# Kernel optimization log

Measured on AMD Instinct MI355X. Metric: run time of the kernel, lower is better.

Reference implementation:

```python
import jax, jax.numpy as jnp
from jax import lax
import numpy as np

B, T, C = 2048, 512, 32  # batch, max_seq_len, num_tags


def setup_inputs() -> dict:
    key = jax.random.key(0)
    k1, k2, k3, k4 = jax.random.split(key, 4)
    logits = jax.random.normal(k1, (B, T, C), dtype=jnp.float32)
    sequence_length = jax.random.randint(k2, (B,), 1, T + 1, dtype=jnp.int32)
    labels = jax.random.randint(k3, (B, T), 0, C, dtype=jnp.int32)
    # learned CRF transition matrix (orthogonal init approximated by normal)
    transitions = jax.random.normal(k4, (C, C), dtype=jnp.float32)
    return dict(logits=logits, sequence_length=sequence_length,
                labels=labels, transitions=transitions)


def _viterbi_decode(logits, transitions, seq_len):
    """tfa_text.crf_decode: returns highest-scoring tag sequence [B, T] int32."""
    Bn, Tn, Cn = logits.shape
    identity_bp = jnp.arange(Cn, dtype=jnp.int32)[None, :]  # carries tag through padding

    def fwd(state, xs):  # state: [B, C] viterbi scores
        logit_t, t = xs
        scores = state[:, :, None] + transitions[None]       # [B, C_prev, C_cur]
        cand = logit_t + jnp.max(scores, axis=1)             # [B, C]
        bp = jnp.argmax(scores, axis=1).astype(jnp.int32)    # [B, C] best prev tag
        active = (t < seq_len)[:, None]
        return (jnp.where(active, cand, state),
                jnp.where(active, bp, identity_bp))

    xs = (jnp.swapaxes(logits[:, 1:], 0, 1), jnp.arange(1, Tn))
    final_state, bps = lax.scan(fwd, logits[:, 0], xs)       # bps: [T-1, B, C]
    last_tag = jnp.argmax(final_state, axis=-1).astype(jnp.int32)  # [B]

    def back(tag, bp):  # tag at t+1 -> tag at t
        prev = jnp.take_along_axis(bp, tag[:, None], axis=1)[:, 0]
        return prev, tag

    first_tag, later_tags = lax.scan(back, last_tag, bps, reverse=True)
    tags = jnp.concatenate([first_tag[None], later_tags], axis=0).T  # [B, T]
    valid = jnp.arange(Tn)[None, :] < seq_len[:, None]
    return jnp.where(valid, tags, 0)


def _crf_log_likelihood(logits, labels, transitions, seq_len):
    """tfa_text.crf_log_likelihood: per-example log-likelihood [B]."""
    Bn, Tn, Cn = logits.shape

    # --- log partition via forward algorithm ---
    def fwd(alpha, xs):
        logit_t, t = xs
        new = jax.nn.logsumexp(alpha[:, :, None] + transitions[None], axis=1) + logit_t
        active = (t < seq_len)[:, None]
        return jnp.where(active, new, alpha), None

    xs = (jnp.swapaxes(logits[:, 1:], 0, 1), jnp.arange(1, Tn))
    alpha, _ = lax.scan(fwd, logits[:, 0], xs)
    log_norm = jax.nn.logsumexp(alpha, axis=-1)  # [B]

    # --- score of gold label sequence ---
    pos = jnp.arange(Tn)
    mask = (pos[None, :] < seq_len[:, None]).astype(logits.dtype)          # [B, T]
    unary = jnp.sum(
        jnp.take_along_axis(logits, labels[..., None], axis=2)[..., 0] * mask,
        axis=1)
    pair_mask = (pos[None, :-1] < (seq_len - 1)[:, None]).astype(logits.dtype)
    binary = jnp.sum(transitions[labels[:, :-1], labels[:, 1:]] * pair_mask, axis=1)

    return unary + binary - log_norm


def reference(logits, sequence_length, labels, transitions):
    # training=True path: labels clamped to >= 0 (already non-negative here)
    labels = jnp.maximum(labels, 0)
    decode_tags = _viterbi_decode(logits, transitions, sequence_length)
    log_likelihood = _crf_log_likelihood(logits, labels, transitions, sequence_length)
    loss = jnp.mean(-log_likelihood)  # recorded via add_loss in the original
    return decode_tags, loss
```

## Files before the change

### kernel.cpp

```cpp
#include <hip/hip_runtime.h>
#include <math.h>

#define BB 2048
#define TT 512
#define CC 32

#if __has_builtin(__builtin_amdgcn_exp2f)
#define EXP2F __builtin_amdgcn_exp2f
#else
#define EXP2F exp2f
#endif
#if __has_builtin(__builtin_amdgcn_logf)
#define LOG2F __builtin_amdgcn_logf
#else
#define LOG2F log2f
#endif

#define LOG2E 1.4426950408889634f
#define LN2   0.6931471805599453f

__global__ void zero_loss_kernel(float* __restrict__ out) {
  if (threadIdx.x == 0) out[(size_t)BB * TT] = 0.0f;
}

#define ROR(dst, src, K)                                                     \
  dst = __int_as_float(__builtin_amdgcn_update_dpp(                          \
      0, __float_as_int(src), 0x120 | (K), 0xF, 0xF, false));

__global__ __launch_bounds__(128, 4) void crf_kernel(
    const float* __restrict__ logits,
    const int*   __restrict__ seqlen,
    const int*   __restrict__ labels,
    const float* __restrict__ trans,
    float*       __restrict__ out)
{
  __shared__ __align__(16) unsigned char bp_s[(TT - 1) * CC];
  __shared__ __align__(16) float avs[CC];
  __shared__ unsigned char tag_s[TT];

  const int lane = threadIdx.x & 63;
  const int wv   = threadIdx.x >> 6;
  const int b    = blockIdx.x;

  const int len = seqlen[b];
  const float* lg = logits + (size_t)b * TT * CC;
  const size_t bT = (size_t)b * TT;

  if (wv == 0) {
    const int c = lane & 31;
    const int h = lane >> 5;

    float tr[16];
#pragma unroll
    for (int i = 0; i < 16; ++i) tr[i] = trans[(h * 16 + i) * CC + c];

    float av = lg[c];
    if (h == 0) avs[c] = av;

    const float4* avp = (const float4*)(avs + h * 16);

    const float* lgc = lg + c;
    float l0 = 0, l1 = 0, l2 = 0;
    {
      int r1 = 1 < len ? 1 : len - 1;
      int r2 = 2 < len ? 2 : len - 1;
      int r3 = 3 < len ? 3 : len - 1;
      l0 = lgc[r1 * CC]; l1 = lgc[r2 * CC]; l2 = lgc[r3 * CC];
    }

    auto vstep = [&](int t, float logit_c) {
      float pav[16];
#pragma unroll
      for (int qq = 0; qq < 4; ++qq) ((float4*)pav)[qq] = avp[qq];

      float S[16];
#pragma unroll
      for (int i = 0; i < 16; ++i) S[i] = pav[i] + tr[i];

      float m8[8];
#pragma unroll
      for (int k = 0; k < 8; ++k) m8[k] = fmaxf(S[k], S[k + 8]);
#pragma unroll
      for (int k = 0; k < 4; ++k) m8[k] = fmaxf(m8[k], m8[k + 4]);
      float best = fmaxf(fmaxf(m8[0], m8[2]), fmaxf(m8[1], m8[3]));

      int t8[16];
#pragma unroll
      for (int i = 0; i < 16; ++i) t8[i] = (S[i] == best) ? i : 63;
#pragma unroll
      for (int k = 0; k < 8; ++k) t8[k] = min(t8[k], t8[k + 8]);
#pragma unroll
      for (int k = 0; k < 4; ++k) t8[k] = min(t8[k], t8[k + 4]);
      int bi = min(min(t8[0], t8[2]), min(t8[1], t8[3]));
      int bpi = h * 16 + bi;

      float ov = __shfl_xor(best, 32);
      int   oi = __shfl_xor(bpi, 32);
      bool take = (ov > best) || (ov == best && oi < bpi);
      best = take ? ov : best;
      bpi  = take ? oi : bpi;
      av = logit_c + best;

      if (h == 0) {
        avs[c] = av;
        bp_s[(t - 1) * CC + c] = (unsigned char)bpi;
      }
    };

    int t = 1;
    int tmain = len - 3;
    for (; t < tmain; ++t) {
      float lc = l0; l0 = l1; l1 = l2;
      l2 = lgc[(t + 3) * CC];
      vstep(t, lc);
    }
    for (; t < len; ++t) {
      float lc = l0; l0 = l1; l1 = l2;
      int rn = t + 3; rn = rn < len ? rn : len - 1;
      l2 = lgc[rn * CC];
      vstep(t, lc);
    }

    float v = av; int idx = c;
#pragma unroll
    for (int d = 1; d < 32; d <<= 1) {
      float v2 = __shfl_xor(v, d, 32);
      int   i2 = __shfl_xor(idx, d, 32);
      if (v2 > v || (v2 == v && i2 < idx)) { v = v2; idx = i2; }
    }

    if (lane == 0) {
      int tag = idx;
      tag_s[len - 1] = (unsigned char)tag;
      const uint4* bp4 = (const uint4*)bp_s;
      uint4 Ra[3], Rb[3];
#pragma unroll
      for (int k = 0; k < 3; ++k) {
        int r = len - 2 - k;
        if (r >= 0) { Ra[k] = bp4[2 * r]; Rb[k] = bp4[2 * r + 1]; }
      }
      for (int tt = len - 1; tt > 0; --tt) {
        uint4 ua = Ra[0], ub = Rb[0];
        Ra[0] = Ra[1]; Rb[0] = Rb[1];
        Ra[1] = Ra[2]; Rb[1] = Rb[2];
        int r = tt - 4;
        if (r >= 0) { Ra[2] = bp4[2 * r]; Rb[2] = bp4[2 * r + 1]; }
        uint4 u4;
        u4.x = (tag & 16) ? ub.x : ua.x;
        u4.y = (tag & 16) ? ub.y : ua.y;
        u4.z = (tag & 16) ? ub.z : ua.z;
        u4.w = (tag & 16) ? ub.w : ua.w;
        unsigned lo = (tag & 8) ? u4.z : u4.x;
        unsigned hi = (tag & 8) ? u4.w : u4.y;
        unsigned u1 = (tag & 4) ? hi : lo;
        tag = (int)((u1 >> ((tag & 3) * 8)) & 0xffu);
        tag_s[tt - 1] = (unsigned char)tag;
      }
    }

#pragma unroll
    for (int j = 0; j < 8; ++j) {
      int tt = lane + 64 * j;
      float val = (tt < len) ? (float)tag_s[tt] : 0.0f;
      out[bT + tt] = val;
    }

  } else {
    const int* lab = labels + (size_t)b * TT;
    const int i = lane & 15;
    const int r = (lane >> 4) & 1;
    const int c = lane & 31;
    const int pr = (lane < 32) ? r : (1 - r);
    const int bpaddr = ((lane < 32) ? lane : (lane ^ 16)) << 2;

    float E[16];
#pragma unroll
    for (int k = 0; k < 16; ++k) {
      int p = pr * 16 + ((i - k) & 15);
      E[k] = EXP2F(trans[p * CC + c] * LOG2E);
    }

    float P   = EXP2F(lg[c] * LOG2E);
    float Acc = 0.0f;

    const float* lgc = lg + c;
    float e0 = 0, e1 = 0, e2 = 0;
    {
      int r1 = 1 < len ? 1 : len - 1;
      int r2 = 2 < len ? 2 : len - 1;
      int r3 = 3 < len ? 3 : len - 1;
      e0 = EXP2F(lgc[r1 * CC] * LOG2E);
      e1 = EXP2F(lgc[r2 * CC] * LOG2E);
      e2 = EXP2F(lgc[r3 * CC] * LOG2E);
    }

    auto fstep = [&](float el) {
      float base = __int_as_float(
          __builtin_amdgcn_ds_bpermute(bpaddr, __float_as_int(P)));
      float x;
      float a0 = base * E[0];
      ROR(x, base, 1);  float a1 = x * E[1];
      ROR(x, base, 2);  float a2 = x * E[2];
      ROR(x, base, 3);  float a3 = x * E[3];
      ROR(x, base, 4);  a0 = fmaf(x, E[4],  a0);
      ROR(x, base, 5);  a1 = fmaf(x, E[5],  a1);
      ROR(x, base, 6);  a2 = fmaf(x, E[6],  a2);
      ROR(x, base, 7);  a3 = fmaf(x, E[7],  a3);
      ROR(x, base, 8);  a0 = fmaf(x, E[8],  a0);
      ROR(x, base, 9);  a1 = fmaf(x, E[9],  a1);
      ROR(x, base, 10); a2 = fmaf(x, E[10], a2);
      ROR(x, base, 11); a3 = fmaf(x, E[11], a3);
      ROR(x, base, 12); a0 = fmaf(x, E[12], a0);
      ROR(x, base, 13); a1 = fmaf(x, E[13], a1);
      ROR(x, base, 14); a2 = fmaf(x, E[14], a2);
      ROR(x, base, 15); a3 = fmaf(x, E[15], a3);
      float part = (a0 + a1) + (a2 + a3);
      float oth  = __shfl_xor(part, 32);
      float s    = part + oth;
      P = el * s;
    };

    auto renorm = [&]() {
      float m = P;
#pragma unroll
      for (int d = 1; d < 32; d <<= 1) m = fmaxf(m, __shfl_xor(m, d, 32));
      int e = (int)(__float_as_uint(m) >> 23) - 127;
      P = ldexpf(P, -e);
      Acc += (float)e;
    };

    int t = 1;
    int tmain = len - 3;
    for (; t < tmain; ++t) {
      float ec = e0; e0 = e1; e1 = e2;
      e2 = EXP2F(lgc[(t + 3) * CC] * LOG2E);
      fstep(ec);
      if ((t & 3) == 0) renorm();
    }
    for (; t < len; ++t) {
      float ec = e0; e0 = e1; e1 = e2;
      int rn = t + 3; rn = rn < len ? rn : len - 1;
      e2 = EXP2F(lgc[rn * CC] * LOG2E);
      fstep(ec);
      if ((t & 3) == 0) renorm();
    }

    float uacc = 0.0f, bacc = 0.0f;
#pragma unroll
    for (int j = 0; j < 8; ++j) {
      int tt = lane + 64 * j;
      if (tt < len) {
        int lt = lab[tt];
        uacc += lg[tt * CC + lt];
        if (tt + 1 < len) {
          int ln = lab[tt + 1];
          bacc += trans[lt * CC + ln];
        }
      }
    }
#pragma unroll
    for (int d = 32; d >= 1; d >>= 1) {
      uacc += __shfl_xor(uacc, d);
      bacc += __shfl_xor(bacc, d);
    }

    float ss = P;
#pragma unroll
    for (int d = 1; d < 32; d <<= 1) ss += __shfl_xor(ss, d, 32);
    float log_norm = LN2 * (Acc + LOG2F(ss));

    if (lane == 0) {
      float ll = uacc + bacc - log_norm;
      atomicAdd(out + (size_t)BB * TT, -ll * (1.0f / BB));
    }
  }
}

extern "C" void kernel_launch(void* const* d_in, const int* in_sizes, int n_in,
                              void* d_out, int out_size, void* d_ws, size_t ws_size,
                              hipStream_t stream) {
  const float* logits = (const float*)d_in[0];
  const int*   seqlen = (const int*)d_in[1];
  const int*   labels = (const int*)d_in[2];
  const float* trans  = (const float*)d_in[3];
  float* out = (float*)d_out;

  zero_loss_kernel<<<1, 64, 0, stream>>>(out);
  crf_kernel<<<dim3(BB), dim3(128), 0, stream>>>(logits, seqlen, labels, trans, out);
}
```

Before: 435.8 us.

## Sort sequences by length and pair long with short per block for load balance

Adds a single-block schedule kernel that counting-sorts batch indices by sequence length in descending order into a workspace permutation. The CRF kernel then launches half as many blocks, and each block processes sequence k and sequence BB-1-k back to back, so every block does roughly equal serial work. This targets the tail imbalance of variable-length sequential scans. It costs an extra tiny kernel launch, serialized sort work, and fewer concurrent blocks, which may lower latency hiding. The new path only runs when a workspace is provided.

```diff
diff --git a/kernel.cpp b/kernel.cpp
--- a/kernel.cpp
+++ b/kernel.cpp
@@ -23,6 +23,31 @@
   if (threadIdx.x == 0) out[(size_t)BB * TT] = 0.0f;
 }
 
+__global__ void schedule_kernel(const int* __restrict__ seqlen,
+                                int* __restrict__ perm,
+                                float* __restrict__ out) {
+  __shared__ int s[TT];
+  __shared__ int off[TT];
+  const int tid = threadIdx.x;
+  if (tid == 0) out[(size_t)BB * TT] = 0.0f;
+  s[tid] = 0;
+  __syncthreads();
+  for (int b = tid; b < BB; b += TT) atomicAdd(&s[seqlen[b] - 1], 1);
+  __syncthreads();
+  for (int d = 1; d < TT; d <<= 1) {
+    int v = s[tid] + ((tid + d < TT) ? s[tid + d] : 0);
+    __syncthreads();
+    s[tid] = v;
+    __syncthreads();
+  }
+  off[tid] = (tid + 1 < TT) ? s[tid + 1] : 0;
+  __syncthreads();
+  for (int b = tid; b < BB; b += TT) {
+    int pos = atomicAdd(&off[seqlen[b] - 1], 1);
+    perm[pos] = b;
+  }
+}
+
 #define ROR(dst, src, K)                                                     \
   dst = __int_as_float(__builtin_amdgcn_update_dpp(                          \
       0, __float_as_int(src), 0x120 | (K), 0xF, 0xF, false));
@@ -32,7 +57,8 @@
     const int*   __restrict__ seqlen,
     const int*   __restrict__ labels,
     const float* __restrict__ trans,
-    float*       __restrict__ out)
+    float*       __restrict__ out,
+    const int*   __restrict__ perm)
 {
   __shared__ __align__(16) unsigned char bp_s[(TT - 1) * CC];
   __shared__ __align__(16) float avs[CC];
@@ -40,11 +66,10 @@
 
   const int lane = threadIdx.x & 63;
   const int wv   = threadIdx.x >> 6;
-  const int b    = blockIdx.x;
-
-  const int len = seqlen[b];
-  const float* lg = logits + (size_t)b * TT * CC;
-  const size_t bT = (size_t)b * TT;
+  const int k    = blockIdx.x;
+
+  const int bs0 = perm ? perm[k] : k;
+  const int bs1 = perm ? perm[BB - 1 - k] : -1;
 
   if (wv == 0) {
     const int c = lane & 31;
@@ -54,119 +79,126 @@
 #pragma unroll
     for (int i = 0; i < 16; ++i) tr[i] = trans[(h * 16 + i) * CC + c];
 
-    float av = lg[c];
-    if (h == 0) avs[c] = av;
-
     const float4* avp = (const float4*)(avs + h * 16);
 
-    const float* lgc = lg + c;
-    float l0 = 0, l1 = 0, l2 = 0;
-    {
-      int r1 = 1 < len ? 1 : len - 1;
-      int r2 = 2 < len ? 2 : len - 1;
-      int r3 = 3 < len ? 3 : len - 1;
-      l0 = lgc[r1 * CC]; l1 = lgc[r2 * CC]; l2 = lgc[r3 * CC];
+    for (int sq = 0; sq < 2; ++sq) {
+      const int b = sq ? bs1 : bs0;
+      if (b < 0) break;
+      const int len = seqlen[b];
+      const float* lg = logits + (size_t)b * TT * CC;
+      const size_t bT = (size_t)b * TT;
+
+      float av = lg[c];
+      if (h == 0) avs[c] = av;
+
+      const float* lgc = lg + c;
+      float l0 = 0, l1 = 0, l2 = 0;
+      {
+        int r1 = 1 < len ? 1 : len - 1;
+        int r2 = 2 < len ? 2 : len - 1;
+        int r3 = 3 < len ? 3 : len - 1;
+        l0 = lgc[r1 * CC]; l1 = lgc[r2 * CC]; l2 = lgc[r3 * CC];
+      }
+
+      auto vstep = [&](int t, float logit_c) {
+        float pav[16];
+#pragma unroll
+        for (int qq = 0; qq < 4; ++qq) ((float4*)pav)[qq] = avp[qq];
+
+        float S[16];
+#pragma unroll
+        for (int i = 0; i < 16; ++i) S[i] = pav[i] + tr[i];
+
+        float m8[8];
+#pragma unroll
+        for (int kk = 0; kk < 8; ++kk) m8[kk] = fmaxf(S[kk], S[kk + 8]);
+#pragma unroll
+        for (int kk = 0; kk < 4; ++kk) m8[kk] = fmaxf(m8[kk], m8[kk + 4]);
+        float best = fmaxf(fmaxf(m8[0], m8[2]), fmaxf(m8[1], m8[3]));
+
+        int t8[16];
+#pragma unroll
+        for (int i = 0; i < 16; ++i) t8[i] = (S[i] == best) ? i : 63;
+#pragma unroll
+        for (int kk = 0; kk < 8; ++kk) t8[kk] = min(t8[kk], t8[kk + 8]);
+#pragma unroll
+        for (int kk = 0; kk < 4; ++kk) t8[kk] = min(t8[kk], t8[kk + 4]);
+        int bi = min(min(t8[0], t8[2]), min(t8[1], t8[3]));
+        int bpi = h * 16 + bi;
+
+        float ov = __shfl_xor(best, 32);
+        int   oi = __shfl_xor(bpi, 32);
+        bool take = (ov > best) || (ov == best && oi < bpi);
+        best = take ? ov : best;
+        bpi  = take ? oi : bpi;
+        av = logit_c + best;
+
+        if (h == 0) {
+          avs[c] = av;
+          bp_s[(t - 1) * CC + c] = (unsigned char)bpi;
+        }
+      };
+
+      int t = 1;
+      int tmain = len - 3;
+      for (; t < tmain; ++t) {
+        float lc = l0; l0 = l1; l1 = l2;
+        l2 = lgc[(t + 3) * CC];
+        vstep(t, lc);
+      }
+      for (; t < len; ++t) {
+        float lc = l0; l0 = l1; l1 = l2;
+        int rn = t + 3; rn = rn < len ? rn : len - 1;
+        l2 = lgc[rn * CC];
+        vstep(t, lc);
+      }
+
+      float v = av; int idx = c;
+#pragma unroll
+      for (int d = 1; d < 32; d <<= 1) {
+        float v2 = __shfl_xor(v, d, 32);
+        int   i2 = __shfl_xor(idx, d, 32);
+        if (v2 > v || (v2 == v && i2 < idx)) { v = v2; idx = i2; }
+      }
+
+      if (lane == 0) {
+        int tag = idx;
+        tag_s[len - 1] = (unsigned char)tag;
+        const uint4* bp4 = (const uint4*)bp_s;
+        uint4 Ra[3], Rb[3];
+#pragma unroll
+        for (int kk = 0; kk < 3; ++kk) {
+          int r = len - 2 - kk;
+          if (r >= 0) { Ra[kk] = bp4[2 * r]; Rb[kk] = bp4[2 * r + 1]; }
+        }
+        for (int tt = len - 1; tt > 0; --tt) {
+          uint4 ua = Ra[0], ub = Rb[0];
+          Ra[0] = Ra[1]; Rb[0] = Rb[1];
+          Ra[1] = Ra[2]; Rb[1] = Rb[2];
+          int r = tt - 4;
+          if (r >= 0) { Ra[2] = bp4[2 * r]; Rb[2] = bp4[2 * r + 1]; }
+          uint4 u4;
+          u4.x = (tag & 16) ? ub.x : ua.x;
+          u4.y = (tag & 16) ? ub.y : ua.y;
+          u4.z = (tag & 16) ? ub.z : ua.z;
+          u4.w = (tag & 16) ? ub.w : ua.w;
+          unsigned lo = (tag & 8) ? u4.z : u4.x;
+          unsigned hi = (tag & 8) ? u4.w : u4.y;
+          unsigned u1 = (tag & 4) ? hi : lo;
+          tag = (int)((u1 >> ((tag & 3) * 8)) & 0xffu);
+          tag_s[tt - 1] = (unsigned char)tag;
+        }
+      }
+
+#pragma unroll
+      for (int j = 0; j < 8; ++j) {
+        int tt = lane + 64 * j;
+        float val = (tt < len) ? (float)tag_s[tt] : 0.0f;
+        out[bT + tt] = val;
+      }
     }
 
-    auto vstep = [&](int t, float logit_c) {
-      float pav[16];
-#pragma unroll
-      for (int qq = 0; qq < 4; ++qq) ((float4*)pav)[qq] = avp[qq];
-
-      float S[16];
-#pragma unroll
-      for (int i = 0; i < 16; ++i) S[i] = pav[i] + tr[i];
-
-      float m8[8];
-#pragma unroll
-      for (int k = 0; k < 8; ++k) m8[k] = fmaxf(S[k], S[k + 8]);
-#pragma unroll
-      for (int k = 0; k < 4; ++k) m8[k] = fmaxf(m8[k], m8[k + 4]);
-      float best = fmaxf(fmaxf(m8[0], m8[2]), fmaxf(m8[1], m8[3]));
-
-      int t8[16];
-#pragma unroll
-      for (int i = 0; i < 16; ++i) t8[i] = (S[i] == best) ? i : 63;
-#pragma unroll
-      for (int k = 0; k < 8; ++k) t8[k] = min(t8[k], t8[k + 8]);
-#pragma unroll
-      for (int k = 0; k < 4; ++k) t8[k] = min(t8[k], t8[k + 4]);
-      int bi = min(min(t8[0], t8[2]), min(t8[1], t8[3]));
-      int bpi = h * 16 + bi;
-
-      float ov = __shfl_xor(best, 32);
-      int   oi = __shfl_xor(bpi, 32);
-      bool take = (ov > best) || (ov == best && oi < bpi);
-      best = take ? ov : best;
-      bpi  = take ? oi : bpi;
-      av = logit_c + best;
-
-      if (h == 0) {
-        avs[c] = av;
-        bp_s[(t - 1) * CC + c] = (unsigned char)bpi;
-      }
-    };
-
-    int t = 1;
-    int tmain = len - 3;
-    for (; t < tmain; ++t) {
-      float lc = l0; l0 = l1; l1 = l2;
-      l2 = lgc[(t + 3) * CC];
-      vstep(t, lc);
-    }
-    for (; t < len; ++t) {
-      float lc = l0; l0 = l1; l1 = l2;
-      int rn = t + 3; rn = rn < len ? rn : len - 1;
-      l2 = lgc[rn * CC];
-      vstep(t, lc);
-    }
-
-    float v = av; int idx = c;
-#pragma unroll
-    for (int d = 1; d < 32; d <<= 1) {
-      float v2 = __shfl_xor(v, d, 32);
-      int   i2 = __shfl_xor(idx, d, 32);
-      if (v2 > v || (v2 == v && i2 < idx)) { v = v2; idx = i2; }
-    }
-
-    if (lane == 0) {
-      int tag = idx;
-      tag_s[len - 1] = (unsigned char)tag;
-      const uint4* bp4 = (const uint4*)bp_s;
-      uint4 Ra[3], Rb[3];
-#pragma unroll
-      for (int k = 0; k < 3; ++k) {
-        int r = len - 2 - k;
-        if (r >= 0) { Ra[k] = bp4[2 * r]; Rb[k] = bp4[2 * r + 1]; }
-      }
-      for (int tt = len - 1; tt > 0; --tt) {
-        uint4 ua = Ra[0], ub = Rb[0];
-        Ra[0] = Ra[1]; Rb[0] = Rb[1];
-        Ra[1] = Ra[2]; Rb[1] = Rb[2];
-        int r = tt - 4;
-        if (r >= 0) { Ra[2] = bp4[2 * r]; Rb[2] = bp4[2 * r + 1]; }
-        uint4 u4;
-        u4.x = (tag & 16) ? ub.x : ua.x;
-        u4.y = (tag & 16) ? ub.y : ua.y;
-        u4.z = (tag & 16) ? ub.z : ua.z;
-        u4.w = (tag & 16) ? ub.w : ua.w;
-        unsigned lo = (tag & 8) ? u4.z : u4.x;
-        unsigned hi = (tag & 8) ? u4.w : u4.y;
-        unsigned u1 = (tag & 4) ? hi : lo;
-        tag = (int)((u1 >> ((tag & 3) * 8)) & 0xffu);
-        tag_s[tt - 1] = (unsigned char)tag;
-      }
-    }
-
-#pragma unroll
-    for (int j = 0; j < 8; ++j) {
-      int tt = lane + 64 * j;
-      float val = (tt < len) ? (float)tag_s[tt] : 0.0f;
-      out[bT + tt] = val;
-    }
-
   } else {
-    const int* lab = labels + (size_t)b * TT;
     const int i = lane & 15;
     const int r = (lane >> 4) & 1;
     const int c = lane & 31;
@@ -175,103 +207,114 @@
 
     float E[16];
 #pragma unroll
-    for (int k = 0; k < 16; ++k) {
-      int p = pr * 16 + ((i - k) & 15);
-      E[k] = EXP2F(trans[p * CC + c] * LOG2E);
+    for (int kk = 0; kk < 16; ++kk) {
+      int p = pr * 16 + ((i - kk) & 15);
+      E[kk] = EXP2F(trans[p * CC + c] * LOG2E);
     }
 
-    float P   = EXP2F(lg[c] * LOG2E);
-    float Acc = 0.0f;
-
-    const float* lgc = lg + c;
-    float e0 = 0, e1 = 0, e2 = 0;
-    {
-      int r1 = 1 < len ? 1 : len - 1;
-      int r2 = 2 < len ? 2 : len - 1;
-      int r3 = 3 < len ? 3 : len - 1;
-      e0 = EXP2F(lgc[r1 * CC] * LOG2E);
-      e1 = EXP2F(lgc[r2 * CC] * LOG2E);
-      e2 = EXP2F(lgc[r3 * CC] * LOG2E);
+    float loss_acc = 0.0f;
+
+    for (int sq = 0; sq < 2; ++sq) {
+      const int b = sq ? bs1 : bs0;
+      if (b < 0) break;
+      const int len = seqlen[b];
+      const float* lg = logits + (size_t)b * TT * CC;
+      const int* lab = labels + (size_t)b * TT;
+
+      float P   = EXP2F(lg[c] * LOG2E);
+      float Acc = 0.0f;
+
+      const float* lgc = lg + c;
+      float e0 = 0, e1 = 0, e2 = 0;
+      {
+        int r1 = 1 < len ? 1 : len - 1;
+        int r2 = 2 < len ? 2 : len - 1;
+        int r3 = 3 < len ? 3 : len - 1;
+        e0 = EXP2F(lgc[r1 * CC] * LOG2E);
+        e1 = EXP2F(lgc[r2 * CC] * LOG2E);
+        e2 = EXP2F(lgc[r3 * CC] * LOG2E);
+      }
+
+      auto fstep = [&](float el) {
+        float base = __int_as_float(
+            __builtin_amdgcn_ds_bpermute(bpaddr, __float_as_int(P)));
+        float x;
+        float a0 = base * E[0];
+        ROR(x, base, 1);  float a1 = x * E[1];
+        ROR(x, base, 2);  float a2 = x * E[2];
+        ROR(x, base, 3);  float a3 = x * E[3];
+        ROR(x, base, 4);  a0 = fmaf(x, E[4],  a0);
+        ROR(x, base, 5);  a1 = fmaf(x, E[5],  a1);
+        ROR(x, base, 6);  a2 = fmaf(x, E[6],  a2);
+        ROR(x, base, 7);  a3 = fmaf(x, E[7],  a3);
+        ROR(x, base, 8);  a0 = fmaf(x, E[8],  a0);
+        ROR(x, base, 9);  a1 = fmaf(x, E[9],  a1);
+        ROR(x, base, 10); a2 = fmaf(x, E[10], a2);
+        ROR(x, base, 11); a3 = fmaf(x, E[11], a3);
+        ROR(x, base, 12); a0 = fmaf(x, E[12], a0);
+        ROR(x, base, 13); a1 = fmaf(x, E[13], a1);
+        ROR(x, base, 14); a2 = fmaf(x, E[14], a2);
+        ROR(x, base, 15); a3 = fmaf(x, E[15], a3);
+        float part = (a0 + a1) + (a2 + a3);
+        float oth  = __shfl_xor(part, 32);
+        float s    = part + oth;
+        P = el * s;
+      };
+
+      auto renorm = [&]() {
+        float m = P;
+#pragma unroll
+        for (int d = 1; d < 32; d <<= 1) m = fmaxf(m, __shfl_xor(m, d, 32));
+        int e = (int)(__float_as_uint(m) >> 23) - 127;
+        P = ldexpf(P, -e);
+        Acc += (float)e;
+      };
+
+      int t = 1;
+      int tmain = len - 3;
+      for (; t < tmain; ++t) {
+        float ec = e0; e0 = e1; e1 = e2;
+        e2 = EXP2F(lgc[(t + 3) * CC] * LOG2E);
+        fstep(ec);
+        if ((t & 3) == 0) renorm();
+      }
+      for (; t < len; ++t) {
+        float ec = e0; e0 = e1; e1 = e2;
+        int rn = t + 3; rn = rn < len ? rn : len - 1;
+        e2 = EXP2F(lgc[rn * CC] * LOG2E);
+        fstep(ec);
+        if ((t & 3) == 0) renorm();
+      }
+
+      float uacc = 0.0f, bacc = 0.0f;
+#pragma unroll
+      for (int j = 0; j < 8; ++j) {
+        int tt = lane + 64 * j;
+        if (tt < len) {
+          int lt = lab[tt];
+          uacc += lg[tt * CC + lt];
+          if (tt + 1 < len) {
+            int ln = lab[tt + 1];
+            bacc += trans[lt * CC + ln];
+          }
+        }
+      }
+#pragma unroll
+      for (int d = 32; d >= 1; d >>= 1) {
+        uacc += __shfl_xor(uacc, d);
+        bacc += __shfl_xor(bacc, d);
+      }
+
+      float ss = P;
+#pragma unroll
+      for (int d = 1; d < 32; d <<= 1) ss += __shfl_xor(ss, d, 32);
+      float log_norm = LN2 * (Acc + LOG2F(ss));
+
+      loss_acc += (uacc + bacc - log_norm);
     }
 
-    auto fstep = [&](float el) {
-      float base = __int_as_float(
-          __builtin_amdgcn_ds_bpermute(bpaddr, __float_as_int(P)));
-      float x;
-      float a0 = base * E[0];
-      ROR(x, base, 1);  float a1 = x * E[1];
-      ROR(x, base, 2);  float a2 = x * E[2];
-      ROR(x, base, 3);  float a3 = x * E[3];
-      ROR(x, base, 4);  a0 = fmaf(x, E[4],  a0);
-      ROR(x, base, 5);  a1 = fmaf(x, E[5],  a1);
-      ROR(x, base, 6);  a2 = fmaf(x, E[6],  a2);
-      ROR(x, base, 7);  a3 = fmaf(x, E[7],  a3);
-      ROR(x, base, 8);  a0 = fmaf(x, E[8],  a0);
-      ROR(x, base, 9);  a1 = fmaf(x, E[9],  a1);
-      ROR(x, base, 10); a2 = fmaf(x, E[10], a2);
-      ROR(x, base, 11); a3 = fmaf(x, E[11], a3);
-      ROR(x, base, 12); a0 = fmaf(x, E[12], a0);
-      ROR(x, base, 13); a1 = fmaf(x, E[13], a1);
-      ROR(x, base, 14); a2 = fmaf(x, E[14], a2);
-      ROR(x, base, 15); a3 = fmaf(x, E[15], a3);
-      float part = (a0 + a1) + (a2 + a3);
-      float oth  = __shfl_xor(part, 32);
-      float s    = part + oth;
-      P = el * s;
-    };
-
-    auto renorm = [&]() {
-      float m = P;
-#pragma unroll
-      for (int d = 1; d < 32; d <<= 1) m = fmaxf(m, __shfl_xor(m, d, 32));
-      int e = (int)(__float_as_uint(m) >> 23) - 127;
-      P = ldexpf(P, -e);
-      Acc += (float)e;
-    };
-
-    int t = 1;
-    int tmain = len - 3;
-    for (; t < tmain; ++t) {
-      float ec = e0; e0 = e1; e1 = e2;
-      e2 = EXP2F(lgc[(t + 3) * CC] * LOG2E);
-      fstep(ec);
-      if ((t & 3) == 0) renorm();
-    }
-    for (; t < len; ++t) {
-      float ec = e0; e0 = e1; e1 = e2;
-      int rn = t + 3; rn = rn < len ? rn : len - 1;
-      e2 = EXP2F(lgc[rn * CC] * LOG2E);
-      fstep(ec);
-      if ((t & 3) == 0) renorm();
-    }
-
-    float uacc = 0.0f, bacc = 0.0f;
-#pragma unroll
-    for (int j = 0; j < 8; ++j) {
-      int tt = lane + 64 * j;
-      if (tt < len) {
-        int lt = lab[tt];
-        uacc += lg[tt * CC + lt];
-        if (tt + 1 < len) {
-          int ln = lab[tt + 1];
-          bacc += trans[lt * CC + ln];
-        }
-      }
-    }
-#pragma unroll
-    for (int d = 32; d >= 1; d >>= 1) {
-      uacc += __shfl_xor(uacc, d);
-      bacc += __shfl_xor(bacc, d);
-    }
-
-    float ss = P;
-#pragma unroll
-    for (int d = 1; d < 32; d <<= 1) ss += __shfl_xor(ss, d, 32);
-    float log_norm = LN2 * (Acc + LOG2F(ss));
-
     if (lane == 0) {
-      float ll = uacc + bacc - log_norm;
-      atomicAdd(out + (size_t)BB * TT, -ll * (1.0f / BB));
+      atomicAdd(out + (size_t)BB * TT, loss_acc * (-1.0f / BB));
     }
   }
 }
@@ -285,6 +328,14 @@
   const float* trans  = (const float*)d_in[3];
   float* out = (float*)d_out;
 
-  zero_loss_kernel<<<1, 64, 0, stream>>>(out);
-  crf_kernel<<<dim3(BB), dim3(128), 0, stream>>>(logits, seqlen, labels, trans, out);
+  if (d_ws != nullptr && ws_size >= BB * sizeof(int)) {
+    int* perm = (int*)d_ws;
+    schedule_kernel<<<1, TT, 0, stream>>>(seqlen, perm, out);
+    crf_kernel<<<dim3(BB / 2), dim3(128), 0, stream>>>(
+        logits, seqlen, labels, trans, out, perm);
+  } else {
+    zero_loss_kernel<<<1, 64, 0, stream>>>(out);
+    crf_kernel<<<dim3(BB), dim3(128), 0, stream>>>(
+        logits, seqlen, labels, trans, out, nullptr);
+  }
 }
```

Result: faster. 421.4 us (-3.3%).
